# Kernel tuning notes

Measured on AMD Instinct MI355X. Metric: run time of the kernel, lower is better.

Reference implementation:

```python
import jax, jax.numpy as jnp
import numpy as np


def _param(k, shape, scale=0.1):
    return (jax.random.normal(k, shape, dtype=jnp.float32) * scale)


def setup_inputs() -> dict:
    key = jax.random.key(0)
    ks = jax.random.split(key, 18)
    B, H, W = 4096, 64, 64
    inp = {
        "x": jax.random.uniform(ks[0], (B, 3, H, W), dtype=jnp.float32),
        # ImprovedColorCombinationHead: mean-RGB -> 128 -> 64 (color_semantic) -> 5 logits
        "clf_w1": _param(ks[1], (3, 128)), "clf_b1": jnp.zeros((128,), jnp.float32),
        "clf_w2": _param(ks[2], (128, 64)), "clf_b2": jnp.zeros((64,), jnp.float32),
        "clf_w3": _param(ks[3], (64, 5)), "clf_b3": jnp.zeros((5,), jnp.float32),
        # ColorRelationReasoning: 8-d one-hot color bins -> 32 (relation_features) -> 5 logits
        "rel_w1": _param(ks[4], (8, 32)), "rel_b1": jnp.zeros((32,), jnp.float32),
        "rel_w2": _param(ks[5], (32, 5)), "rel_b2": jnp.zeros((5,), jnp.float32),
        # integration_layer: Linear(10,64) ReLU Linear(64,32) ReLU Linear(32,5) (dropout=eval/identity)
        "int_w1": _param(ks[6], (10, 64)), "int_b1": jnp.zeros((64,), jnp.float32),
        "int_w2": _param(ks[7], (64, 32)), "int_b2": jnp.zeros((32,), jnp.float32),
        "int_w3": _param(ks[8], (32, 5)), "int_b3": jnp.zeros((5,), jnp.float32),
        "classifier_weight": jnp.asarray(0.7, jnp.float32),
        "reasoner_weight": jnp.asarray(0.3, jnp.float32),
    }
    return inp


def _color_bins(mean_rgb):
    # Vectorized replacement of the per-sample Python binning loop.
    r, g, b = mean_rgb[:, 0], mean_rgb[:, 1], mean_rgb[:, 2]
    conds = jnp.stack([
        (r > 0.5) & (g < 0.3) & (b < 0.3),   # red
        (r > 0.5) & (g > 0.3) & (b < 0.3),   # orange
        (r > 0.5) & (g > 0.5) & (b < 0.3),   # yellow (shadowed by prev, kept for fidelity)
        (r < 0.3) & (g > 0.5) & (b < 0.3),   # green
        (r < 0.3) & (g < 0.3) & (b > 0.5),   # blue
        (r > 0.5) & (g < 0.3) & (b > 0.5),   # magenta
        (r > 0.7) & (g > 0.7) & (b > 0.7),   # white
        (r < 0.3) & (g < 0.3) & (b < 0.3),   # black
    ], axis=0)                                # [8, B]
    any_hit = jnp.any(conds, axis=0)
    first_hit = jnp.argmax(conds, axis=0)           # first-true index = elif priority order
    fallback = jnp.argmax(mean_rgb, axis=1)         # else branch: one-hot at argmax channel (0..2)
    idx = jnp.where(any_hit, first_hit, fallback)
    return jax.nn.one_hot(idx, 8, dtype=mean_rgb.dtype)  # [B, 8]


def reference(x, clf_w1, clf_b1, clf_w2, clf_b2, clf_w3, clf_b3,
              rel_w1, rel_b1, rel_w2, rel_b2,
              int_w1, int_b1, int_w2, int_b2, int_w3, int_b3,
              classifier_weight, reasoner_weight):
    mean_rgb = jnp.mean(x, axis=(2, 3))                       # [B, 3]
    # classifier head
    h = jax.nn.relu(mean_rgb @ clf_w1 + clf_b1)
    color_semantic = jax.nn.relu(h @ clf_w2 + clf_b2)          # [B, 64]
    classifier_logits = color_semantic @ clf_w3 + clf_b3       # [B, 5]
    classifier_probs = jax.nn.softmax(classifier_logits, axis=-1)
    # relation reasoner over binned color features
    color_features = _color_bins(mean_rgb)                     # [B, 8]
    relation_features = jax.nn.relu(color_features @ rel_w1 + rel_b1)  # [B, 32]
    relation_logits = relation_features @ rel_w2 + rel_b2      # [B, 5]
    relation_probs = jax.nn.softmax(relation_logits, axis=-1)
    # integration MLP (dropout in eval mode = identity)
    combined = jnp.concatenate([classifier_probs, relation_probs], axis=-1)  # [B, 10]
    ih = jax.nn.relu(combined @ int_w1 + int_b1)
    ih = jax.nn.relu(ih @ int_w2 + int_b2)
    integrated_logits = ih @ int_w3 + int_b3
    integrated_probs = jax.nn.softmax(integrated_logits, axis=-1)
    # weighted final fusion
    final_logits = classifier_weight * classifier_logits + reasoner_weight * relation_logits
    final_probs = jax.nn.softmax(final_logits, axis=-1)
    # [B, 20]: all four prob heads concatenated
    return jnp.concatenate([classifier_probs, relation_probs, integrated_probs, final_probs], axis=-1)
```

## Files before the change

kernel.cpp:

```cpp
#include <hip/hip_runtime.h>


typedef float f4 __attribute__((ext_vector_type(4)));

__device__ __forceinline__ void softmax5(const float* __restrict__ in, float* __restrict__ out) {
    float m = in[0];
#pragma unroll
    for (int i = 1; i < 5; ++i) m = fmaxf(m, in[i]);
    float e[5];
    float s = 0.f;
#pragma unroll
    for (int i = 0; i < 5; ++i) { e[i] = expf(in[i] - m); s += e[i]; }
#pragma unroll
    for (int i = 0; i < 5; ++i) out[i] = e[i] / s;
}

extern "C" __global__ void __launch_bounds__(256)
mean_kernel(const float* __restrict__ x, float* __restrict__ means)
{
    __shared__ double s_wsum[3][4];
    const int tid = threadIdx.x;
    const int b   = blockIdx.x;

    const f4* xb = reinterpret_cast<const f4*>(x + (size_t)b * 12288);
    double s0 = 0.0, s1 = 0.0, s2 = 0.0;
#pragma unroll
    for (int k = 0; k < 4; ++k) {
        f4 v0 = __builtin_nontemporal_load(xb + tid + k * 256);
        f4 v1 = __builtin_nontemporal_load(xb + 1024 + tid + k * 256);
        f4 v2 = __builtin_nontemporal_load(xb + 2048 + tid + k * 256);
        s0 += (double)v0.x + (double)v0.y + (double)v0.z + (double)v0.w;
        s1 += (double)v1.x + (double)v1.y + (double)v1.z + (double)v1.w;
        s2 += (double)v2.x + (double)v2.y + (double)v2.z + (double)v2.w;
    }
#pragma unroll
    for (int off = 32; off > 0; off >>= 1) {
        s0 += __shfl_down(s0, off);
        s1 += __shfl_down(s1, off);
        s2 += __shfl_down(s2, off);
    }
    const int wid = tid >> 6;
    if ((tid & 63) == 0) { s_wsum[0][wid] = s0; s_wsum[1][wid] = s1; s_wsum[2][wid] = s2; }
    __syncthreads();
    if (tid < 3) {
        double t = (s_wsum[tid][0] + s_wsum[tid][1]) + (s_wsum[tid][2] + s_wsum[tid][3]);
        means[b * 3 + tid] = (float)(t * (1.0 / 4096.0));
    }
}

extern "C" __global__ void __launch_bounds__(192)
mlp_kernel(const float* __restrict__ means,
           const float* __restrict__ cw1, const float* __restrict__ cb1,
           const float* __restrict__ cw2, const float* __restrict__ cb2,
           const float* __restrict__ cw3, const float* __restrict__ cb3,
           const float* __restrict__ rw1, const float* __restrict__ rb1,
           const float* __restrict__ rw2, const float* __restrict__ rb2,
           const float* __restrict__ iw1, const float* __restrict__ ib1,
           const float* __restrict__ iw2, const float* __restrict__ ib2,
           const float* __restrict__ iw3, const float* __restrict__ ib3,
           const float* __restrict__ cwgt, const float* __restrict__ rwgt,
           float* __restrict__ out)
{
    __shared__ float  s_mean[3];
    __shared__ float  s_h[128];
    __shared__ float  s_cs[64];
    __shared__ float  s_clfl[5];
    __shared__ float  s_rell[5];
    __shared__ float  s_cf[8];
    __shared__ float  s_rf[32];
    __shared__ float  s_ih[64];
    __shared__ float  s_ih2[32];
    __shared__ float  s_intl[5];
    __shared__ float  s_finl[5];
    __shared__ float  s_outp[20];

    const int tid = threadIdx.x;
    const int b   = blockIdx.x;

    if (tid < 3) s_mean[tid] = means[b * 3 + tid];
    __syncthreads();

    if (tid < 128) {
        float a = cb1[tid]
                + s_mean[0] * cw1[tid]
                + s_mean[1] * cw1[128 + tid]
                + s_mean[2] * cw1[256 + tid];
        s_h[tid] = fmaxf(a, 0.f);
    } else if (tid == 128) {
        const float r = s_mean[0], g = s_mean[1], bl = s_mean[2];
        int idx;
        if      (r > 0.5f && g < 0.3f && bl < 0.3f) idx = 0;
        else if (r > 0.5f && g > 0.3f && bl < 0.3f) idx = 1;
        else if (r > 0.5f && g > 0.5f && bl < 0.3f) idx = 2;
        else if (r < 0.3f && g > 0.5f && bl < 0.3f) idx = 3;
        else if (r < 0.3f && g < 0.3f && bl > 0.5f) idx = 4;
        else if (r > 0.5f && g < 0.3f && bl > 0.5f) idx = 5;
        else if (r > 0.7f && g > 0.7f && bl > 0.7f) idx = 6;
        else if (r < 0.3f && g < 0.3f && bl < 0.3f) idx = 7;
        else {
            idx = 0; float m = r;
            if (g  > m) { m = g;  idx = 1; }
            if (bl > m) { m = bl; idx = 2; }
        }
#pragma unroll
        for (int j = 0; j < 8; ++j) s_cf[j] = (j == idx) ? 1.f : 0.f;
    }
    __syncthreads();

    if (tid < 64) {
        float a = cb2[tid];
        for (int k = 0; k < 128; ++k) a += s_h[k] * cw2[k * 64 + tid];
        s_cs[tid] = fmaxf(a, 0.f);
    } else if (tid >= 64 && tid < 96) {
        const int j = tid - 64;
        float a = rb1[j];
#pragma unroll
        for (int k = 0; k < 8; ++k) a += s_cf[k] * rw1[k * 32 + j];
        s_rf[j] = fmaxf(a, 0.f);
    }
    __syncthreads();

    if (tid < 5) {
        float a = cb3[tid];
        for (int k = 0; k < 64; ++k) a += s_cs[k] * cw3[k * 5 + tid];
        s_clfl[tid] = a;
    } else if (tid >= 32 && tid < 37) {
        const int j = tid - 32;
        float a = rb2[j];
        for (int k = 0; k < 32; ++k) a += s_rf[k] * rw2[k * 5 + j];
        s_rell[j] = a;
    }
    __syncthreads();

    if (tid == 0)       softmax5(s_clfl, s_outp);
    else if (tid == 64) softmax5(s_rell, s_outp + 5);
    __syncthreads();

    if (tid < 64) {
        float a = ib1[tid];
#pragma unroll
        for (int k = 0; k < 10; ++k) a += s_outp[k] * iw1[k * 64 + tid];
        s_ih[tid] = fmaxf(a, 0.f);
    }
    __syncthreads();

    if (tid < 32) {
        float a = ib2[tid];
        for (int k = 0; k < 64; ++k) a += s_ih[k] * iw2[k * 32 + tid];
        s_ih2[tid] = fmaxf(a, 0.f);
    } else if (tid >= 32 && tid < 37) {
        const int j = tid - 32;
        s_finl[j] = cwgt[0] * s_clfl[j] + rwgt[0] * s_rell[j];
    }
    __syncthreads();

    if (tid < 5) {
        float a = ib3[tid];
        for (int k = 0; k < 32; ++k) a += s_ih2[k] * iw3[k * 5 + tid];
        s_intl[tid] = a;
    }
    __syncthreads();

    if (tid == 0)       softmax5(s_intl, s_outp + 10);
    else if (tid == 64) softmax5(s_finl, s_outp + 15);
    __syncthreads();

    if (tid < 20) out[(size_t)b * 20 + tid] = s_outp[tid];
}

extern "C" __global__ void __launch_bounds__(256)
icrm_fused(const float* __restrict__ x,
           const float* __restrict__ cw1, const float* __restrict__ cb1,
           const float* __restrict__ cw2, const float* __restrict__ cb2,
           const float* __restrict__ cw3, const float* __restrict__ cb3,
           const float* __restrict__ rw1, const float* __restrict__ rb1,
           const float* __restrict__ rw2, const float* __restrict__ rb2,
           const float* __restrict__ iw1, const float* __restrict__ ib1,
           const float* __restrict__ iw2, const float* __restrict__ ib2,
           const float* __restrict__ iw3, const float* __restrict__ ib3,
           const float* __restrict__ cwgt, const float* __restrict__ rwgt,
           float* __restrict__ out)
{
    __shared__ float  s_mean[3];
    __shared__ float  s_h[128];
    __shared__ float  s_cs[64];
    __shared__ float  s_clfl[5];
    __shared__ float  s_rell[5];
    __shared__ float  s_cf[8];
    __shared__ float  s_rf[32];
    __shared__ float  s_ih[64];
    __shared__ float  s_ih2[32];
    __shared__ float  s_intl[5];
    __shared__ float  s_finl[5];
    __shared__ float  s_outp[20];
    __shared__ double s_wsum[3][4];

    const int tid = threadIdx.x;
    const int b   = blockIdx.x;

    const float4* xb = reinterpret_cast<const float4*>(x + (size_t)b * 12288);
    double s0 = 0.0, s1 = 0.0, s2 = 0.0;
#pragma unroll
    for (int k = 0; k < 4; ++k) {
        float4 v0 = xb[tid + k * 256];
        float4 v1 = xb[1024 + tid + k * 256];
        float4 v2 = xb[2048 + tid + k * 256];
        s0 += (double)v0.x + (double)v0.y + (double)v0.z + (double)v0.w;
        s1 += (double)v1.x + (double)v1.y + (double)v1.z + (double)v1.w;
        s2 += (double)v2.x + (double)v2.y + (double)v2.z + (double)v2.w;
    }
#pragma unroll
    for (int off = 32; off > 0; off >>= 1) {
        s0 += __shfl_down(s0, off);
        s1 += __shfl_down(s1, off);
        s2 += __shfl_down(s2, off);
    }
    const int wid = tid >> 6;
    if ((tid & 63) == 0) { s_wsum[0][wid] = s0; s_wsum[1][wid] = s1; s_wsum[2][wid] = s2; }
    __syncthreads();
    if (tid < 3) {
        double t = (s_wsum[tid][0] + s_wsum[tid][1]) + (s_wsum[tid][2] + s_wsum[tid][3]);
        s_mean[tid] = (float)(t * (1.0 / 4096.0));
    }
    __syncthreads();

    if (tid < 128) {
        float a = cb1[tid]
                + s_mean[0] * cw1[tid]
                + s_mean[1] * cw1[128 + tid]
                + s_mean[2] * cw1[256 + tid];
        s_h[tid] = fmaxf(a, 0.f);
    } else if (tid == 128) {
        const float r = s_mean[0], g = s_mean[1], bl = s_mean[2];
        int idx;
        if      (r > 0.5f && g < 0.3f && bl < 0.3f) idx = 0;
        else if (r > 0.5f && g > 0.3f && bl < 0.3f) idx = 1;
        else if (r > 0.5f && g > 0.5f && bl < 0.3f) idx = 2;
        else if (r < 0.3f && g > 0.5f && bl < 0.3f) idx = 3;
        else if (r < 0.3f && g < 0.3f && bl > 0.5f) idx = 4;
        else if (r > 0.5f && g < 0.3f && bl > 0.5f) idx = 5;
        else if (r > 0.7f && g > 0.7f && bl > 0.7f) idx = 6;
        else if (r < 0.3f && g < 0.3f && bl < 0.3f) idx = 7;
        else {
            idx = 0; float m = r;
            if (g  > m) { m = g;  idx = 1; }
            if (bl > m) { m = bl; idx = 2; }
        }
#pragma unroll
        for (int j = 0; j < 8; ++j) s_cf[j] = (j == idx) ? 1.f : 0.f;
    }
    __syncthreads();

    if (tid < 64) {
        float a = cb2[tid];
        for (int k = 0; k < 128; ++k) a += s_h[k] * cw2[k * 64 + tid];
        s_cs[tid] = fmaxf(a, 0.f);
    } else if (tid >= 64 && tid < 96) {
        const int j = tid - 64;
        float a = rb1[j];
#pragma unroll
        for (int k = 0; k < 8; ++k) a += s_cf[k] * rw1[k * 32 + j];
        s_rf[j] = fmaxf(a, 0.f);
    }
    __syncthreads();

    if (tid < 5) {
        float a = cb3[tid];
        for (int k = 0; k < 64; ++k) a += s_cs[k] * cw3[k * 5 + tid];
        s_clfl[tid] = a;
    } else if (tid >= 32 && tid < 37) {
        const int j = tid - 32;
        float a = rb2[j];
        for (int k = 0; k < 32; ++k) a += s_rf[k] * rw2[k * 5 + j];
        s_rell[j] = a;
    }
    __syncthreads();

    if (tid == 0)       softmax5(s_clfl, s_outp);
    else if (tid == 64) softmax5(s_rell, s_outp + 5);
    __syncthreads();

    if (tid < 64) {
        float a = ib1[tid];
#pragma unroll
        for (int k = 0; k < 10; ++k) a += s_outp[k] * iw1[k * 64 + tid];
        s_ih[tid] = fmaxf(a, 0.f);
    }
    __syncthreads();

    if (tid < 32) {
        float a = ib2[tid];
        for (int k = 0; k < 64; ++k) a += s_ih[k] * iw2[k * 32 + tid];
        s_ih2[tid] = fmaxf(a, 0.f);
    } else if (tid >= 32 && tid < 37) {
        const int j = tid - 32;
        s_finl[j] = cwgt[0] * s_clfl[j] + rwgt[0] * s_rell[j];
    }
    __syncthreads();

    if (tid < 5) {
        float a = ib3[tid];
        for (int k = 0; k < 32; ++k) a += s_ih2[k] * iw3[k * 5 + tid];
        s_intl[tid] = a;
    }
    __syncthreads();

    if (tid == 0)       softmax5(s_intl, s_outp + 10);
    else if (tid == 64) softmax5(s_finl, s_outp + 15);
    __syncthreads();

    if (tid < 20) out[(size_t)b * 20 + tid] = s_outp[tid];
}

extern "C" void kernel_launch(void* const* d_in, const int* in_sizes, int n_in,
                              void* d_out, int out_size, void* d_ws, size_t ws_size,
                              hipStream_t stream) {
    const float* x    = (const float*)d_in[0];
    const float* cw1  = (const float*)d_in[1];
    const float* cb1  = (const float*)d_in[2];
    const float* cw2  = (const float*)d_in[3];
    const float* cb2  = (const float*)d_in[4];
    const float* cw3  = (const float*)d_in[5];
    const float* cb3  = (const float*)d_in[6];
    const float* rw1  = (const float*)d_in[7];
    const float* rb1  = (const float*)d_in[8];
    const float* rw2  = (const float*)d_in[9];
    const float* rb2  = (const float*)d_in[10];
    const float* iw1  = (const float*)d_in[11];
    const float* ib1  = (const float*)d_in[12];
    const float* iw2  = (const float*)d_in[13];
    const float* ib2  = (const float*)d_in[14];
    const float* iw3  = (const float*)d_in[15];
    const float* ib3  = (const float*)d_in[16];
    const float* cwgt = (const float*)d_in[17];
    const float* rwgt = (const float*)d_in[18];
    float* out = (float*)d_out;

    const int B = in_sizes[0] / (3 * 64 * 64);

    if (ws_size >= (size_t)B * 3 * sizeof(float)) {
        float* means = (float*)d_ws;
        mean_kernel<<<B, 256, 0, stream>>>(x, means);
        mlp_kernel<<<B, 192, 0, stream>>>(means, cw1, cb1, cw2, cb2, cw3, cb3,
                                          rw1, rb1, rw2, rb2,
                                          iw1, ib1, iw2, ib2, iw3, ib3,
                                          cwgt, rwgt, out);
    } else {
        icrm_fused<<<B, 256, 0, stream>>>(x, cw1, cb1, cw2, cb2, cw3, cb3,
                                          rw1, rb1, rw2, rb2,
                                          iw1, ib1, iw2, ib2, iw3, ib3,
                                          cwgt, rwgt, out);
    }
}
```

Measured before the change: 51.68 us.

## Replace per-sample mean kernel with persistent lockstep plane-sweeping reduction

The per-sample mean kernel (4096 blocks of 256 threads) is replaced by 512 blocks of 1024 threads. Each block walks 24 channel planes in lockstep, so all blocks read nearby addresses at the same time, and it prefetches the next plane while reducing the current one. The intent is to make the DRAM access pattern more sequential and cut block launch overhead. In exchange, each plane needs two block-wide barriers and each thread has only one load in flight, which may limit memory-level parallelism. The fast path is hardcoded to B==4096.

```diff
diff --git a/kernel.cpp b/kernel.cpp
--- a/kernel.cpp
+++ b/kernel.cpp
@@ -15,36 +15,43 @@
     for (int i = 0; i < 5; ++i) out[i] = e[i] / s;
 }
 
-extern "C" __global__ void __launch_bounds__(256)
-mean_kernel(const float* __restrict__ x, float* __restrict__ means)
+extern "C" __global__ void __launch_bounds__(1024)
+mean_lockstep(const float* __restrict__ x, float* __restrict__ means)
 {
-    __shared__ double s_wsum[3][4];
-    const int tid = threadIdx.x;
-    const int b   = blockIdx.x;
-
-    const f4* xb = reinterpret_cast<const f4*>(x + (size_t)b * 12288);
-    double s0 = 0.0, s1 = 0.0, s2 = 0.0;
-#pragma unroll
-    for (int k = 0; k < 4; ++k) {
-        f4 v0 = __builtin_nontemporal_load(xb + tid + k * 256);
-        f4 v1 = __builtin_nontemporal_load(xb + 1024 + tid + k * 256);
-        f4 v2 = __builtin_nontemporal_load(xb + 2048 + tid + k * 256);
-        s0 += (double)v0.x + (double)v0.y + (double)v0.z + (double)v0.w;
-        s1 += (double)v1.x + (double)v1.y + (double)v1.z + (double)v1.w;
-        s2 += (double)v2.x + (double)v2.y + (double)v2.z + (double)v2.w;
-    }
-#pragma unroll
-    for (int off = 32; off > 0; off >>= 1) {
-        s0 += __shfl_down(s0, off);
-        s1 += __shfl_down(s1, off);
-        s2 += __shfl_down(s2, off);
-    }
-    const int wid = tid >> 6;
-    if ((tid & 63) == 0) { s_wsum[0][wid] = s0; s_wsum[1][wid] = s1; s_wsum[2][wid] = s2; }
-    __syncthreads();
-    if (tid < 3) {
-        double t = (s_wsum[tid][0] + s_wsum[tid][1]) + (s_wsum[tid][2] + s_wsum[tid][3]);
-        means[b * 3 + tid] = (float)(t * (1.0 / 4096.0));
+    __shared__ double part[16];
+    const int tid  = threadIdx.x;
+    const int lane = tid & 63;
+    const int w    = tid >> 6;
+    const int i    = blockIdx.x;
+
+    const f4* x4 = reinterpret_cast<const f4*>(x);
+
+    f4 v = x4[(size_t)i * 1024 + tid];
+
+#pragma unroll
+    for (int k = 0; k < 24; ++k) {
+        f4 vn;
+        if (k < 23) vn = x4[((size_t)(k + 1) * 512 + i) * 1024 + tid];
+
+        double s = ((double)v.x + (double)v.y) + ((double)v.z + (double)v.w);
+#pragma unroll
+        for (int off = 32; off > 0; off >>= 1) s += __shfl_down(s, off);
+        if (lane == 0) part[w] = s;
+
+        asm volatile("s_waitcnt lgkmcnt(0)" ::: "memory");
+        __builtin_amdgcn_s_barrier();
+        __builtin_amdgcn_sched_barrier(0);
+
+        if (w == 0) {
+            double t = (lane < 16) ? part[lane] : 0.0;
+#pragma unroll
+            for (int off = 8; off > 0; off >>= 1) t += __shfl_down(t, off);
+            if (lane == 0) means[k * 512 + i] = (float)(t * (1.0 / 4096.0));
+        }
+        __builtin_amdgcn_s_barrier();
+        __builtin_amdgcn_sched_barrier(0);
+
+        v = vn;
     }
 }
 
@@ -338,9 +345,9 @@
 
     const int B = in_sizes[0] / (3 * 64 * 64);
 
-    if (ws_size >= (size_t)B * 3 * sizeof(float)) {
+    if (B == 4096 && ws_size >= (size_t)B * 3 * sizeof(float)) {
         float* means = (float*)d_ws;
-        mean_kernel<<<B, 256, 0, stream>>>(x, means);
+        mean_lockstep<<<512, 1024, 0, stream>>>(x, means);
         mlp_kernel<<<B, 192, 0, stream>>>(means, cw1, cb1, cw2, cb2, cw3, cb3,
                                           rw1, rb1, rw2, rb2,
                                           iw1, ib1, iw2, ib2, iw3, ib3,
```

Result: slower. 61.66 us (+19.3%).
